# Optimization experiments

Measured on AMD Instinct MI355X. Metric: run time of the kernel, lower is better.

## Reference

```python
import jax, jax.numpy as jnp
import numpy as np

K = 3  # kernel size (hardcoded in module defaults; padding=1, stride=1, dilation=1)


def conv2d(x, w, b, pad=1):
    # x: [B,C,H,W], w: [O,C,kh,kw]
    out = jax.lax.conv_general_dilated(
        x, w, window_strides=(1, 1), padding=[(pad, pad), (pad, pad)],
        dimension_numbers=("NCHW", "OIHW", "NCHW"))
    return out + b[None, :, None, None]


def _bilinear_sample(img, py, px):
    # img: [C,H,W]; py, px: [K*K,Ho,Wo] float sample coords.
    # Zero-padded bilinear sampling (matches torchvision deform_conv2d):
    # each of the 4 corner taps contributes 0 if it lies outside the image.
    H, W = img.shape[1], img.shape[2]
    y0 = jnp.floor(py)
    x0 = jnp.floor(px)
    y1, x1 = y0 + 1.0, x0 + 1.0
    wy1 = py - y0
    wy0 = 1.0 - wy1
    wx1 = px - x0
    wx0 = 1.0 - wx1

    def corner(y, x):
        yi = jnp.clip(y.astype(jnp.int32), 0, H - 1)
        xi = jnp.clip(x.astype(jnp.int32), 0, W - 1)
        valid = ((y >= 0) & (y <= H - 1) & (x >= 0) & (x <= W - 1))
        return img[:, yi, xi] * valid.astype(img.dtype)[None]  # [C,K*K,Ho,Wo]

    return (corner(y0, x0) * (wy0 * wx0)[None]
            + corner(y0, x1) * (wy0 * wx1)[None]
            + corner(y1, x0) * (wy1 * wx0)[None]
            + corner(y1, x1) * (wy1 * wx1)[None])


def setup_inputs() -> dict:
    key = jax.random.key(0)
    ks = jax.random.split(key, 4)
    B, C, O, H, W = 8, 128, 256, 96, 96
    x = jax.random.normal(ks[0], (B, C, H, W), dtype=jnp.float32)
    # scale offset/mask conv weights so learned offsets stay a few pixels
    offset_w = jax.random.normal(ks[1], (2 * K * K, C, K, K), dtype=jnp.float32) * 0.01
    offset_b = jnp.zeros((2 * K * K,), dtype=jnp.float32)
    mask_w = jax.random.normal(ks[2], (K * K, C, K, K), dtype=jnp.float32) * 0.05
    mask_b = jnp.zeros((K * K,), dtype=jnp.float32)
    weight = jax.random.normal(ks[3], (O, C, K, K), dtype=jnp.float32) * 0.05
    bias = jnp.zeros((O,), dtype=jnp.float32)
    return {"x": x, "offset_w": offset_w, "offset_b": offset_b,
            "mask_w": mask_w, "mask_b": mask_b, "weight": weight, "bias": bias}


def reference(x, offset_w, offset_b, mask_w, mask_b, weight, bias):
    B, C, H, W = x.shape
    O = weight.shape[0]
    pad = 1
    offset = conv2d(x, offset_w, offset_b, pad)              # [B,2*K*K,H,W]
    mask = jax.nn.sigmoid(conv2d(x, mask_w, mask_b, pad))    # [B,K*K,H,W]
    Ho, Wo = offset.shape[2], offset.shape[3]

    # base sampling grid: output pixel - pad + kernel tap position
    kh, kw = jnp.meshgrid(jnp.arange(K), jnp.arange(K), indexing="ij")
    kh = kh.reshape(-1).astype(x.dtype)  # [K*K]
    kw = kw.reshape(-1).astype(x.dtype)
    base_y = (jnp.arange(Ho, dtype=x.dtype)[None, :, None] - pad
              + kh[:, None, None])                           # [K*K,Ho,1]
    base_x = (jnp.arange(Wo, dtype=x.dtype)[None, None, :] - pad
              + kw[:, None, None])                           # [K*K,1,Wo]

    # torchvision layout: channel 2k = y-offset, 2k+1 = x-offset for tap k
    off = offset.reshape(B, K * K, 2, Ho, Wo)
    py = base_y[None] + off[:, :, 0]                         # [B,K*K,Ho,Wo]
    px = base_x[None] + off[:, :, 1]

    samples = jax.vmap(_bilinear_sample)(x, py, px)          # [B,C,K*K,Ho,Wo]
    w_flat = weight.reshape(O, C, K * K)
    out = jnp.einsum("bckhw,bkhw,ock->bohw", samples, mask, w_flat)
    return out + bias[None, :, None, None]
```

## Files before the change

### kernel.cpp

```cpp
#include <hip/hip_runtime.h>

#define CIN 128
#define COUT 256
#define IH 96
#define IW 96
#define NB 8
#define HW (IH*IW)
#define NPIX (NB*HW)
#define AST 136
#define BLK_PER_IMG (HW/64)

typedef __attribute__((ext_vector_type(8))) short short8;
typedef __attribute__((ext_vector_type(4))) float floatx4;

static __device__ __forceinline__ short f2bf(float f) {
  unsigned int u = __builtin_bit_cast(unsigned int, f);
  u = u + 0x7fffu + ((u >> 16) & 1u);
  return (short)(u >> 16);
}
static __device__ __forceinline__ float bf2f(short s) {
  unsigned int u = ((unsigned int)(unsigned short)s) << 16;
  return __builtin_bit_cast(float, u);
}

struct Corner {
  float w00, w01, w10, w11;
  const short *r00, *r01, *r10, *r11;
};

static __device__ __forceinline__ Corner corner_setup(float py, float px, float mk,
                                                      const short* xtb, int choff) {
  Corner c;
  float y0f = floorf(py), x0f = floorf(px);
  float wy1 = py - y0f, wx1 = px - x0f;
  float wy0 = 1.f - wy1, wx0 = 1.f - wx1;
  bool vy0 = (y0f >= 0.f) && (y0f <= (float)(IH - 1));
  bool vy1 = (y0f + 1.f >= 0.f) && (y0f + 1.f <= (float)(IH - 1));
  bool vx0 = (x0f >= 0.f) && (x0f <= (float)(IW - 1));
  bool vx1 = (x0f + 1.f >= 0.f) && (x0f + 1.f <= (float)(IW - 1));
  int iy0 = min(max((int)y0f, 0), IH - 1);
  int iy1 = min(max((int)y0f + 1, 0), IH - 1);
  int ix0 = min(max((int)x0f, 0), IW - 1);
  int ix1 = min(max((int)x0f + 1, 0), IW - 1);
  c.w00 = wy0 * wx0 * mk * ((vy0 && vx0) ? 1.f : 0.f);
  c.w01 = wy0 * wx1 * mk * ((vy0 && vx1) ? 1.f : 0.f);
  c.w10 = wy1 * wx0 * mk * ((vy1 && vx0) ? 1.f : 0.f);
  c.w11 = wy1 * wx1 * mk * ((vy1 && vx1) ? 1.f : 0.f);
  c.r00 = xtb + (size_t)(iy0 * IW + ix0) * 128 + choff;
  c.r01 = xtb + (size_t)(iy0 * IW + ix1) * 128 + choff;
  c.r10 = xtb + (size_t)(iy1 * IW + ix0) * 128 + choff;
  c.r11 = xtb + (size_t)(iy1 * IW + ix1) * 128 + choff;
  return c;
}

static __device__ __forceinline__ short8 interp8(short8 s00, short8 s01,
                                                 short8 s10, short8 s11,
                                                 const Corner& c) {
  short8 o;
  #pragma unroll
  for (int j = 0; j < 8; ++j) {
    float v = c.w00 * bf2f(s00[j]) + c.w01 * bf2f(s01[j])
            + c.w10 * bf2f(s10[j]) + c.w11 * bf2f(s11[j]);
    o[j] = f2bf(v);
  }
  return o;
}

__global__ void prep_weights(const float* __restrict__ weight,
                             const float* __restrict__ offset_w,
                             const float* __restrict__ mask_w,
                             short* __restrict__ Bt2f,
                             short* __restrict__ Bt1f) {
  int idx = blockIdx.x * 256 + threadIdx.x;
  const int n2 = 9 * 4 * 16 * 512;
  if (idx < n2) {
    int e = idx & 7, lane = (idx >> 3) & 63;
    int g = idx >> 9;
    int nl = g & 15, kq = (g >> 4) & 3, tap = g >> 6;
    int o = nl * 16 + (lane & 15);
    int c = kq * 32 + (lane >> 4) * 8 + e;
    Bt2f[idx] = f2bf(weight[(o * CIN + c) * 9 + tap]);
  } else {
    int j = idx - n2;
    if (j < 9 * 4 * 2 * 512) {
      int e = j & 7, lane = (j >> 3) & 63;
      int g = j >> 9;
      int nl = g & 1, kq = (g >> 1) & 3, tap = g >> 3;
      int n = nl * 16 + (lane & 15);
      int c = kq * 32 + (lane >> 4) * 8 + e;
      float v = 0.f;
      if (n < 27)
        v = (n < 18) ? offset_w[(n * CIN + c) * 9 + tap]
                     : mask_w[((n - 18) * CIN + c) * 9 + tap];
      Bt1f[j] = f2bf(v);
    }
  }
}

__global__ __launch_bounds__(256, 8)
void transpose_x(const float* __restrict__ x, short* __restrict__ xt) {
  __shared__ short tile[64 * 130];
  const int tid = threadIdx.x;
  const int lane = tid & 63;
  const int wv = tid >> 6;
  const int p0 = blockIdx.x * 64;
  const int b = p0 / HW;
  const int hw0 = p0 % HW;
  const float* xb = x + (size_t)b * CIN * HW + hw0;

  #pragma unroll
  for (int i = 0; i < 32; ++i) {
    int c = wv + i * 4;
    tile[lane * 130 + c] = f2bf(xb[(size_t)c * HW + lane]);
  }
  __syncthreads();

  unsigned int* dst = (unsigned int*)(xt + ((size_t)b * HW + hw0) * 128);
  #pragma unroll
  for (int i = 0; i < 16; ++i) {
    int idx = i * 256 + tid;
    int px = idx >> 6, cw = idx & 63;
    unsigned int lo = (unsigned short)tile[px * 130 + 2 * cw];
    unsigned int hi = (unsigned short)tile[px * 130 + 2 * cw + 1];
    dst[idx] = lo | (hi << 16);
  }
}

__global__ __launch_bounds__(256, 3)
void deform_main(const short* __restrict__ xt,
                 const short* __restrict__ Bt2f,
                 const short* __restrict__ Bt1f,
                 const float* __restrict__ offset_b,
                 const float* __restrict__ mask_b,
                 const float* __restrict__ bias,
                 float* __restrict__ out) {
  __shared__ short Ald[2][64 * AST];
  __shared__ float pmb[27 * 65];

  const int tid  = threadIdx.x;
  const int lane = tid & 63;
  const int wv   = tid >> 6;
  const int q    = lane >> 4;
  const int m    = lane & 15;
  const int blk  = blockIdx.x;
  const int l    = (blk & 7) * BLK_PER_IMG + (blk >> 3);
  const int p0   = l * 64;
  const int b    = p0 / HW;
  const short* xtb = xt + (size_t)b * HW * 128;

  {
    const int p  = p0 + wv * 16 + m;
    const int hw = p % HW;
    const int h  = hw / IW, w_ = hw % IW;

    floatx4 acc0 = (floatx4){0.f, 0.f, 0.f, 0.f};
    floatx4 acc1 = (floatx4){0.f, 0.f, 0.f, 0.f};

    for (int tap = 0; tap < 9; ++tap) {
      const int kh = tap / 3, kw = tap % 3;
      const int iy = h + kh - 1, ix = w_ + kw - 1;
      const bool vald = (iy >= 0 && iy < IH && ix >= 0 && ix < IW);
      const size_t pbase = vald ? (size_t)(iy * IW + ix) * 128 : 0;

      short8 a[4], bb0[4], bb1[4];
      #pragma unroll
      for (int kq = 0; kq < 4; ++kq)
        a[kq] = *(const short8*)(xtb + pbase + kq * 32 + q * 8);
      #pragma unroll
      for (int kq = 0; kq < 4; ++kq) {
        bb0[kq] = *(const short8*)(Bt1f + (size_t)((tap * 4 + kq) * 2 + 0) * 512 + lane * 8);
        bb1[kq] = *(const short8*)(Bt1f + (size_t)((tap * 4 + kq) * 2 + 1) * 512 + lane * 8);
      }
      #pragma unroll
      for (int kq = 0; kq < 4; ++kq) {
        short8 av = a[kq];
        if (!vald) av = (short8){0, 0, 0, 0, 0, 0, 0, 0};
        acc0 = __builtin_amdgcn_mfma_f32_16x16x32_bf16(av, bb0[kq], acc0, 0, 0, 0);
        acc1 = __builtin_amdgcn_mfma_f32_16x16x32_bf16(av, bb1[kq], acc1, 0, 0, 0);
      }
    }

    #pragma unroll
    for (int nl = 0; nl < 2; ++nl) {
      floatx4 ac = nl ? acc1 : acc0;
      int ch = nl * 16 + m;
      if (ch < 18) {
        int tap = ch >> 1, plane = ch & 1;
        float cb = offset_b[ch];
        #pragma unroll
        for (int r = 0; r < 4; ++r) {
          int col = wv * 16 + q * 4 + r;
          int hwp = (p0 + col) % HW;
          float base = plane ? (float)(hwp % IW + tap % 3 - 1)
                             : (float)(hwp / IW + tap / 3 - 1);
          pmb[(plane * 9 + tap) * 65 + col] = ac[r] + cb + base;
        }
      } else if (ch < 27) {
        int tap = ch - 18;
        float cb = mask_b[tap];
        #pragma unroll
        for (int r = 0; r < 4; ++r) {
          int col = wv * 16 + q * 4 + r;
          float v = ac[r] + cb;
          pmb[(18 + tap) * 65 + col] = 1.f / (1.f + expf(-v));
        }
      }
    }
  }
  __syncthreads();

  const int r8    = lane >> 3;
  const int ck    = lane & 7;
  const int ckoff = ck * 8;
  const int row0  = wv * 16 + r8;
  const int row1  = row0 + 8;
  const int wk0   = (row0 >> 1) & 7;
  const int wk1   = (row1 >> 1) & 7;
  const int wb0   = row0 * AST;
  const int wb1   = row1 * AST;
  const int rsw   = (m >> 1) & 7;

  floatx4 acc[4][4];
  #pragma unroll
  for (int i = 0; i < 4; ++i)
    #pragma unroll
    for (int j = 0; j < 4; ++j) acc[i][j] = (floatx4){0.f, 0.f, 0.f, 0.f};

  {
    float py0 = pmb[row0], px0 = pmb[9 * 65 + row0], mk0 = pmb[18 * 65 + row0];
    float py1 = pmb[row1], px1 = pmb[9 * 65 + row1], mk1 = pmb[18 * 65 + row1];
    Corner c0 = corner_setup(py0, px0, mk0, xtb, ckoff);
    Corner c1 = corner_setup(py1, px1, mk1, xtb, ckoff);
    short8 a0 = *(const short8*)(c0.r00),      a1 = *(const short8*)(c0.r01);
    short8 a2 = *(const short8*)(c0.r10),      a3 = *(const short8*)(c0.r11);
    short8 a4 = *(const short8*)(c0.r00 + 64), a5 = *(const short8*)(c0.r01 + 64);
    short8 a6 = *(const short8*)(c0.r10 + 64), a7 = *(const short8*)(c0.r11 + 64);
    short8 b0 = *(const short8*)(c1.r00),      b1 = *(const short8*)(c1.r01);
    short8 b2 = *(const short8*)(c1.r10),      b3 = *(const short8*)(c1.r11);
    short8 b4 = *(const short8*)(c1.r00 + 64), b5 = *(const short8*)(c1.r01 + 64);
    short8 b6 = *(const short8*)(c1.r10 + 64), b7 = *(const short8*)(c1.r11 + 64);
    *(short8*)(&Ald[0][wb0 + (ck ^ wk0) * 8])       = interp8(a0, a1, a2, a3, c0);
    *(short8*)(&Ald[0][wb0 + (8 + (ck ^ wk0)) * 8]) = interp8(a4, a5, a6, a7, c0);
    *(short8*)(&Ald[0][wb1 + (ck ^ wk1) * 8])       = interp8(b0, b1, b2, b3, c1);
    *(short8*)(&Ald[0][wb1 + (8 + (ck ^ wk1)) * 8]) = interp8(b4, b5, b6, b7, c1);
  }
  float pyN0 = pmb[1 * 65 + row0];
  float pxN0 = pmb[10 * 65 + row0];
  float mkN0 = pmb[19 * 65 + row0];
  float pyN1 = pmb[1 * 65 + row1];
  float pxN1 = pmb[10 * 65 + row1];
  float mkN1 = pmb[19 * 65 + row1];
  __syncthreads();

  for (int tap = 0; tap < 9; ++tap) {
    const short* bufr = Ald[tap & 1];
    short* const wbuf = Ald[(tap & 1) ^ 1];
    const bool nxt = (tap < 8);

    Corner c0, c1;
    if (nxt) {
      c0 = corner_setup(pyN0, pxN0, mkN0, xtb, ckoff);
      c1 = corner_setup(pyN1, pxN1, mkN1, xtb, ckoff);
    }
    if (tap < 7) {
      pyN0 = pmb[(tap + 2) * 65 + row0];
      pxN0 = pmb[(tap + 11) * 65 + row0];
      mkN0 = pmb[(tap + 20) * 65 + row0];
      pyN1 = pmb[(tap + 2) * 65 + row1];
      pxN1 = pmb[(tap + 11) * 65 + row1];
      mkN1 = pmb[(tap + 20) * 65 + row1];
    }

    short8 bfA[4], bfB[4];
    #pragma unroll
    for (int nl = 0; nl < 4; ++nl) {
      bfA[nl] = *(const short8*)(Bt2f + (size_t)((tap * 4 + 0) * 16 + wv * 4 + nl) * 512 + lane * 8);
      bfB[nl] = *(const short8*)(Bt2f + (size_t)((tap * 4 + 1) * 16 + wv * 4 + nl) * 512 + lane * 8);
    }
    short8 g0, g1, g2, g3, g4, g5, g6, g7;
    if (nxt) {
      g0 = *(const short8*)(c0.r00);      g1 = *(const short8*)(c0.r01);
      g2 = *(const short8*)(c0.r10);      g3 = *(const short8*)(c0.r11);
      g4 = *(const short8*)(c0.r00 + 64); g5 = *(const short8*)(c0.r01 + 64);
      g6 = *(const short8*)(c0.r10 + 64); g7 = *(const short8*)(c0.r11 + 64);
    }
    {
      short8 af[4];
      #pragma unroll
      for (int mt = 0; mt < 4; ++mt)
        af[mt] = *(const short8*)(bufr + (mt * 16 + m) * AST + ((0 * 4 + q) ^ rsw) * 8);
      #pragma unroll
      for (int mt = 0; mt < 4; ++mt)
        #pragma unroll
        for (int nl = 0; nl < 4; ++nl)
          acc[mt][nl] = __builtin_amdgcn_mfma_f32_16x16x32_bf16(af[mt], bfA[nl], acc[mt][nl], 0, 0, 0);
    }
    {
      short8 af[4];
      #pragma unroll
      for (int mt = 0; mt < 4; ++mt)
        af[mt] = *(const short8*)(bufr + (mt * 16 + m) * AST + ((1 * 4 + q) ^ rsw) * 8);
      #pragma unroll
      for (int mt = 0; mt < 4; ++mt)
        #pragma unroll
        for (int nl = 0; nl < 4; ++nl)
          acc[mt][nl] = __builtin_amdgcn_mfma_f32_16x16x32_bf16(af[mt], bfB[nl], acc[mt][nl], 0, 0, 0);
    }
    short8 bfC[4], bfD[4];
    #pragma unroll
    for (int nl = 0; nl < 4; ++nl) {
      bfC[nl] = *(const short8*)(Bt2f + (size_t)((tap * 4 + 2) * 16 + wv * 4 + nl) * 512 + lane * 8);
      bfD[nl] = *(const short8*)(Bt2f + (size_t)((tap * 4 + 3) * 16 + wv * 4 + nl) * 512 + lane * 8);
    }
    if (nxt) {
      *(short8*)(&wbuf[wb0 + (ck ^ wk0) * 8])       = interp8(g0, g1, g2, g3, c0);
      *(short8*)(&wbuf[wb0 + (8 + (ck ^ wk0)) * 8]) = interp8(g4, g5, g6, g7, c0);
      g0 = *(const short8*)(c1.r00);      g1 = *(const short8*)(c1.r01);
      g2 = *(const short8*)(c1.r10);      g3 = *(const short8*)(c1.r11);
      g4 = *(const short8*)(c1.r00 + 64); g5 = *(const short8*)(c1.r01 + 64);
      g6 = *(const short8*)(c1.r10 + 64); g7 = *(const short8*)(c1.r11 + 64);
    }
    {
      short8 af[4];
      #pragma unroll
      for (int mt = 0; mt < 4; ++mt)
        af[mt] = *(const short8*)(bufr + (mt * 16 + m) * AST + ((2 * 4 + q) ^ rsw) * 8);
      #pragma unroll
      for (int mt = 0; mt < 4; ++mt)
        #pragma unroll
        for (int nl = 0; nl < 4; ++nl)
          acc[mt][nl] = __builtin_amdgcn_mfma_f32_16x16x32_bf16(af[mt], bfC[nl], acc[mt][nl], 0, 0, 0);
    }
    {
      short8 af[4];
      #pragma unroll
      for (int mt = 0; mt < 4; ++mt)
        af[mt] = *(const short8*)(bufr + (mt * 16 + m) * AST + ((3 * 4 + q) ^ rsw) * 8);
      #pragma unroll
      for (int mt = 0; mt < 4; ++mt)
        #pragma unroll
        for (int nl = 0; nl < 4; ++nl)
          acc[mt][nl] = __builtin_amdgcn_mfma_f32_16x16x32_bf16(af[mt], bfD[nl], acc[mt][nl], 0, 0, 0);
    }
    if (nxt) {
      *(short8*)(&wbuf[wb1 + (ck ^ wk1) * 8])       = interp8(g0, g1, g2, g3, c1);
      *(short8*)(&wbuf[wb1 + (8 + (ck ^ wk1)) * 8]) = interp8(g4, g5, g6, g7, c1);
      __syncthreads();
    }
  }

  const int hw0 = p0 % HW;
  #pragma unroll
  for (int nl = 0; nl < 4; ++nl) {
    const int o = wv * 64 + nl * 16 + m;
    const float bs = bias[o];
    float* op = out + (size_t)(b * COUT + o) * HW + hw0;
    #pragma unroll
    for (int mt = 0; mt < 4; ++mt) {
      floatx4 v = acc[mt][nl];
      v[0] += bs; v[1] += bs; v[2] += bs; v[3] += bs;
      *(floatx4*)(op + mt * 16 + q * 4) = v;
    }
  }
}

extern "C" void kernel_launch(void* const* d_in, const int* in_sizes, int n_in,
                              void* d_out, int out_size, void* d_ws, size_t ws_size,
                              hipStream_t stream) {
  const float* x        = (const float*)d_in[0];
  const float* offset_w = (const float*)d_in[1];
  const float* offset_b = (const float*)d_in[2];
  const float* mask_w   = (const float*)d_in[3];
  const float* mask_b   = (const float*)d_in[4];
  const float* weight   = (const float*)d_in[5];
  const float* bias     = (const float*)d_in[6];
  float* out = (float*)d_out;

  char* ws = (char*)d_ws;
  const size_t XT_BYTES  = (size_t)NPIX * 128 * 2;
  const size_t BT2_BYTES = (size_t)9 * 4 * 16 * 512 * 2;
  short* xtp  = (short*)ws;
  short* Bt2f = (short*)(ws + XT_BYTES);
  short* Bt1f = (short*)(ws + XT_BYTES + BT2_BYTES);

  prep_weights<<<dim3(1296), dim3(256), 0, stream>>>(weight, offset_w, mask_w, Bt2f, Bt1f);
  transpose_x<<<dim3(NPIX / 64), dim3(256), 0, stream>>>(x, xtp);
  deform_main<<<dim3(NPIX / 64), dim3(256), 0, stream>>>(xtp, Bt2f, Bt1f, offset_b, mask_b, bias, out);
}
```

Baseline: 221.4 us.

## Fuse weight prep into transpose kernel and vectorize transpose loads/stores

Merges the weight-prep kernel into the input transpose kernel as extra blocks, which removes one kernel launch and lets both run concurrently. The transpose now loads float4 from two channels at a time, packs bf16 pairs into 32-bit LDS writes, and writes global memory as uint4 instead of 32-bit words. The aim is fewer memory instructions and less launch overhead in the preprocessing stage. The main kernel is unchanged, so any gain is limited to the prep phase.

```diff
diff --git a/kernel.cpp b/kernel.cpp
--- a/kernel.cpp
+++ b/kernel.cpp
@@ -9,6 +9,7 @@
 #define NPIX (NB*HW)
 #define AST 136
 #define BLK_PER_IMG (HW/64)
+#define TBLK (NPIX/64)
 
 typedef __attribute__((ext_vector_type(8))) short short8;
 typedef __attribute__((ext_vector_type(4))) float floatx4;
@@ -66,63 +67,81 @@
   return o;
 }
 
-__global__ void prep_weights(const float* __restrict__ weight,
-                             const float* __restrict__ offset_w,
-                             const float* __restrict__ mask_w,
-                             short* __restrict__ Bt2f,
-                             short* __restrict__ Bt1f) {
-  int idx = blockIdx.x * 256 + threadIdx.x;
-  const int n2 = 9 * 4 * 16 * 512;
-  if (idx < n2) {
-    int e = idx & 7, lane = (idx >> 3) & 63;
-    int g = idx >> 9;
-    int nl = g & 15, kq = (g >> 4) & 3, tap = g >> 6;
-    int o = nl * 16 + (lane & 15);
-    int c = kq * 32 + (lane >> 4) * 8 + e;
-    Bt2f[idx] = f2bf(weight[(o * CIN + c) * 9 + tap]);
-  } else {
-    int j = idx - n2;
-    if (j < 9 * 4 * 2 * 512) {
-      int e = j & 7, lane = (j >> 3) & 63;
-      int g = j >> 9;
-      int nl = g & 1, kq = (g >> 1) & 3, tap = g >> 3;
-      int n = nl * 16 + (lane & 15);
-      int c = kq * 32 + (lane >> 4) * 8 + e;
-      float v = 0.f;
-      if (n < 27)
-        v = (n < 18) ? offset_w[(n * CIN + c) * 9 + tap]
-                     : mask_w[((n - 18) * CIN + c) * 9 + tap];
-      Bt1f[j] = f2bf(v);
-    }
-  }
-}
-
 __global__ __launch_bounds__(256, 8)
-void transpose_x(const float* __restrict__ x, short* __restrict__ xt) {
+void prep_and_transpose(const float* __restrict__ x, short* __restrict__ xt,
+                        const float* __restrict__ weight,
+                        const float* __restrict__ offset_w,
+                        const float* __restrict__ mask_w,
+                        short* __restrict__ Bt2f, short* __restrict__ Bt1f) {
+  const int blk = blockIdx.x;
+  const int tid = threadIdx.x;
+
+  if (blk >= TBLK) {
+    const int n2 = 9 * 4 * 16 * 512;
+    int base = (blk - TBLK) * 1024 + tid;
+    #pragma unroll
+    for (int k = 0; k < 4; ++k) {
+      int idx = base + k * 256;
+      if (idx < n2) {
+        int e = idx & 7, lane = (idx >> 3) & 63;
+        int g = idx >> 9;
+        int nl = g & 15, kq = (g >> 4) & 3, tap = g >> 6;
+        int o = nl * 16 + (lane & 15);
+        int c = kq * 32 + (lane >> 4) * 8 + e;
+        Bt2f[idx] = f2bf(weight[(o * CIN + c) * 9 + tap]);
+      } else {
+        int j = idx - n2;
+        int e = j & 7, lane = (j >> 3) & 63;
+        int g = j >> 9;
+        int nl = g & 1, kq = (g >> 1) & 3, tap = g >> 3;
+        int n = nl * 16 + (lane & 15);
+        int c = kq * 32 + (lane >> 4) * 8 + e;
+        float v = 0.f;
+        if (n < 27)
+          v = (n < 18) ? offset_w[(n * CIN + c) * 9 + tap]
+                       : mask_w[((n - 18) * CIN + c) * 9 + tap];
+        Bt1f[j] = f2bf(v);
+      }
+    }
+    return;
+  }
+
   __shared__ short tile[64 * 130];
-  const int tid = threadIdx.x;
-  const int lane = tid & 63;
-  const int wv = tid >> 6;
-  const int p0 = blockIdx.x * 64;
-  const int b = p0 / HW;
+  const int p0  = blk * 64;
+  const int b   = p0 / HW;
   const int hw0 = p0 % HW;
   const float* xb = x + (size_t)b * CIN * HW + hw0;
 
+  const int pq = tid & 15;
+  const int cg = tid >> 4;
+
   #pragma unroll
-  for (int i = 0; i < 32; ++i) {
-    int c = wv + i * 4;
-    tile[lane * 130 + c] = f2bf(xb[(size_t)c * HW + lane]);
+  for (int r = 0; r < 4; ++r) {
+    const int c = r * 32 + cg * 2;
+    float4 v0 = *(const float4*)(xb + (size_t)c * HW + 4 * pq);
+    float4 v1 = *(const float4*)(xb + (size_t)(c + 1) * HW + 4 * pq);
+    unsigned int d0 = (unsigned short)f2bf(v0.x) | ((unsigned int)(unsigned short)f2bf(v1.x) << 16);
+    unsigned int d1 = (unsigned short)f2bf(v0.y) | ((unsigned int)(unsigned short)f2bf(v1.y) << 16);
+    unsigned int d2 = (unsigned short)f2bf(v0.z) | ((unsigned int)(unsigned short)f2bf(v1.z) << 16);
+    unsigned int d3 = (unsigned short)f2bf(v0.w) | ((unsigned int)(unsigned short)f2bf(v1.w) << 16);
+    *(unsigned int*)(&tile[(4 * pq + 0) * 130 + c]) = d0;
+    *(unsigned int*)(&tile[(4 * pq + 1) * 130 + c]) = d1;
+    *(unsigned int*)(&tile[(4 * pq + 2) * 130 + c]) = d2;
+    *(unsigned int*)(&tile[(4 * pq + 3) * 130 + c]) = d3;
   }
   __syncthreads();
 
   unsigned int* dst = (unsigned int*)(xt + ((size_t)b * HW + hw0) * 128);
   #pragma unroll
-  for (int i = 0; i < 16; ++i) {
-    int idx = i * 256 + tid;
-    int px = idx >> 6, cw = idx & 63;
-    unsigned int lo = (unsigned short)tile[px * 130 + 2 * cw];
-    unsigned int hi = (unsigned short)tile[px * 130 + 2 * cw + 1];
-    dst[idx] = lo | (hi << 16);
+  for (int i = 0; i < 4; ++i) {
+    int gidx = i * 1024 + tid * 4;
+    int px = gidx >> 6, cw0 = gidx & 63;
+    uint4 w;
+    w.x = *(const unsigned int*)(&tile[px * 130 + 2 * (cw0 + 0)]);
+    w.y = *(const unsigned int*)(&tile[px * 130 + 2 * (cw0 + 1)]);
+    w.z = *(const unsigned int*)(&tile[px * 130 + 2 * (cw0 + 2)]);
+    w.w = *(const unsigned int*)(&tile[px * 130 + 2 * (cw0 + 3)]);
+    *(uint4*)(dst + gidx) = w;
   }
 }
 
@@ -383,7 +402,8 @@
   short* Bt2f = (short*)(ws + XT_BYTES);
   short* Bt1f = (short*)(ws + XT_BYTES + BT2_BYTES);
 
-  prep_weights<<<dim3(1296), dim3(256), 0, stream>>>(weight, offset_w, mask_w, Bt2f, Bt1f);
-  transpose_x<<<dim3(NPIX / 64), dim3(256), 0, stream>>>(x, xtp);
-  deform_main<<<dim3(NPIX / 64), dim3(256), 0, stream>>>(xtp, Bt2f, Bt1f, offset_b, mask_b, bias, out);
-}
+  prep_and_transpose<<<dim3(TBLK + 324), dim3(256), 0, stream>>>(
+      x, xtp, weight, offset_w, mask_w, Bt2f, Bt1f);
+  deform_main<<<dim3(NPIX / 64), dim3(256), 0, stream>>>(
+      xtp, Bt2f, Bt1f, offset_b, mask_b, bias, out);
+}
```

Result: no change. 217.6 us (-1.7%).
